# Kernel tuning notes

Measured on AMD Instinct MI355X. Metric: run time of the kernel, lower is better.

Reference implementation:

```python
import jax, jax.numpy as jnp
import numpy as np

LN_EPS = 1e-3  # keras LayerNormalization default epsilon

def setup_inputs() -> dict:
    key = jax.random.key(0)
    ks = jax.random.split(key, 8)
    B, T, N, F_in, F_out, S = 4, 4, 65536, 16, 32, 8
    E = 589824  # ~9 edges per node (8-neighbor grid + self loop)
    return {
        "water": jax.random.normal(ks[0], (B, T, N, F_in), jnp.float32),
        "static": jax.random.uniform(ks[1], (B, T, N, S), jnp.float32),
        "adj_rows": jax.random.randint(ks[2], (E,), 0, N, jnp.int32),
        "adj_cols": jax.random.randint(ks[3], (E,), 0, N, jnp.int32),
        "adj_vals": jax.random.uniform(ks[4], (E,), jnp.float32),
        "W_feat": (jax.random.normal(ks[5], (F_in, F_out), jnp.float32) * 0.1),
        "b_feat": jnp.zeros((F_out,), jnp.float32),
        "Wg1": (jax.random.normal(ks[6], (3, 1), jnp.float32) * 0.1),
        "bg1": jnp.zeros((1,), jnp.float32),
        "Wg2": (jax.random.normal(ks[7], (S - 3, 1), jnp.float32) * 0.1),
        "bg2": jnp.zeros((1,), jnp.float32),
        "ln_gamma": jnp.ones((F_out,), jnp.float32),
        "ln_beta": jnp.zeros((F_out,), jnp.float32),
        "min_gate": jnp.float32(0.1),
    }


def reference(water, static, adj_rows, adj_cols, adj_vals,
              W_feat, b_feat, Wg1, bg1, Wg2, bg2, ln_gamma, ln_beta, min_gate):
    B, T, N, F_in = water.shape
    # gated feature scaling: gate in (0,1], per (b,t,n)
    gate = jax.nn.sigmoid(static[..., :3] @ Wg1 + bg1) * jax.nn.sigmoid(static[..., 3:] @ Wg2 + bg2)
    gate = jnp.maximum(gate, min_gate)  # [B,T,N,1]
    x = (water * gate).reshape(B * T, N, F_in)
    # SpMM shared across all F_in channels and all B*T slices:
    # out[bt,n,f] = sum_{edges (n<-m)} adj_vals * x[bt,m,f]
    xs = x.transpose(1, 0, 2)                       # [N, BT, F]
    msg = adj_vals[:, None, None] * xs[adj_cols]    # [E, BT, F]
    agg = jax.ops.segment_sum(msg, adj_rows, num_segments=N)  # [N, BT, F]
    h = agg.transpose(1, 0, 2)                      # [BT, N, F]
    out = h @ W_feat + b_feat                       # [BT, N, F_out]
    out = out.reshape(B, T, N, -1)
    # layer norm over channel axis (keras default axis=-1)
    mu = out.mean(-1, keepdims=True)
    var = out.var(-1, keepdims=True)
    out = (out - mu) * jax.lax.rsqrt(var + LN_EPS) * ln_gamma + ln_beta
    # dropout is identity at inference
    return out
```

## Files before the change

### kernel.cpp

```cpp
#include <hip/hip_runtime.h>

#define BT   16
#define FIN  16
#define FOUT 32
#define CAP  32

typedef float    f32x4 __attribute__((ext_vector_type(4)));
typedef _Float16 f16x4 __attribute__((ext_vector_type(4)));
typedef _Float16 f16x8 __attribute__((ext_vector_type(8)));
typedef unsigned int u32;


__global__ __launch_bounds__(256) void zero_kernel(int4* __restrict__ p, int n4) {
    int i = blockIdx.x * 256 + threadIdx.x;
    if (i < n4) p[i] = make_int4(0, 0, 0, 0);
}


__global__ __launch_bounds__(256) void scatter_gate_kernel(
        const int* __restrict__ rows, const int* __restrict__ cols,
        const float* __restrict__ vals,
        int* __restrict__ cur, u32* __restrict__ edge_s, int E, int eb,
        const float* __restrict__ water,
        const float* __restrict__ st,
        const float* __restrict__ Wg1, const float* __restrict__ bg1,
        const float* __restrict__ Wg2, const float* __restrict__ bg2,
        const float* __restrict__ min_gate,
        _Float16* __restrict__ x, int N) {
    if (blockIdx.x < (unsigned)eb) {
        int i0 = (blockIdx.x * 256 + threadIdx.x) * 4;
        if (i0 + 4 <= E) {
            int4   r4 = *(const int4*)  (rows + i0);
            int4   c4 = *(const int4*)  (cols + i0);
            f32x4  v4 = *(const f32x4*) (vals + i0);
#pragma unroll
            for (int k = 0; k < 4; ++k) {
                int r = (&r4.x)[k];
                int pos = atomicAdd(&cur[r], 1);
                unsigned short vh = __builtin_bit_cast(unsigned short, (_Float16)v4[k]);
                if (pos < CAP)
                    edge_s[(size_t)r * CAP + pos] = ((u32)vh << 16) | (u32)(&c4.x)[k];
            }
        } else {
            for (int e = i0; e < E; ++e) {
                int r = rows[e];
                int pos = atomicAdd(&cur[r], 1);
                unsigned short vh = __builtin_bit_cast(unsigned short, (_Float16)vals[e]);
                if (pos < CAP)
                    edge_s[(size_t)r * CAP + pos] = ((u32)vh << 16) | (u32)cols[e];
            }
        }
    } else {
        int g  = blockIdx.x - eb;
        int n  = g * 16 + (threadIdx.x & 15);
        int bt = threadIdx.x >> 4;

        const f32x4* sp = (const f32x4*)(st + ((size_t)bt * N + n) * 8);
        f32x4 s0 = __builtin_nontemporal_load(sp);
        f32x4 s1 = __builtin_nontemporal_load(sp + 1);
        float g1 = s0.x * Wg1[0] + s0.y * Wg1[1] + s0.z * Wg1[2] + bg1[0];
        float g2 = s0.w * Wg2[0] + s1.x * Wg2[1] + s1.y * Wg2[2] + s1.z * Wg2[3] + s1.w * Wg2[4] + bg2[0];
        g1 = 1.f / (1.f + __expf(-g1));
        g2 = 1.f / (1.f + __expf(-g2));
        float gate = fmaxf(g1 * g2, min_gate[0]);

        const f32x4* wp = (const f32x4*)(water + ((size_t)bt * N + n) * FIN);
        f16x8 h0, h1;
#pragma unroll
        for (int k = 0; k < 4; ++k) {
            f32x4 w = __builtin_nontemporal_load(wp + k);
            w *= gate;
            f16x8& h = (k < 2) ? h0 : h1;
            int b = (k & 1) * 4;
            h[b + 0] = (_Float16)w.x; h[b + 1] = (_Float16)w.y;
            h[b + 2] = (_Float16)w.z; h[b + 3] = (_Float16)w.w;
        }
        f16x8* xp = (f16x8*)(x + ((size_t)n * BT + bt) * FIN);
        xp[0] = h0;
        xp[1] = h1;
    }
}


#define GATHER(i, off)                                                           \
    u32 p##i = ebase[e + off];                                                   \
    f16x4 g##i = xv[(size_t)(p##i & 0xffffu) * 64 + l];

#define EDGE_FMA(i)                                                              \
    do {                                                                         \
        float v = (float)__builtin_bit_cast(_Float16, (unsigned short)(p##i >> 16)); \
        acc.x += v * (float)g##i[0];                                             \
        acc.y += v * (float)g##i[1];                                             \
        acc.z += v * (float)g##i[2];                                             \
        acc.w += v * (float)g##i[3];                                             \
    } while (0)

__global__ __launch_bounds__(256) void spmm_ln_kernel(
        const _Float16* __restrict__ x,
        const int* __restrict__ cur,
        const u32* __restrict__ edge_s,
        const float* __restrict__ W,
        const float* __restrict__ bvec,
        const float* __restrict__ gamma,
        const float* __restrict__ beta,
        float* __restrict__ out, int N) {
    __shared__ float Wsh[FIN][FOUT];
    __shared__ float psh[3][FOUT];

    int t = threadIdx.x;
    Wsh[t >> 5][t & 31]       = W[t];
    Wsh[(t >> 5) + 8][t & 31] = W[t + 256];
    if (t < 32)       psh[0][t]      = bvec[t];
    else if (t < 64)  psh[1][t - 32] = gamma[t - 32];
    else if (t < 96)  psh[2][t - 64] = beta[t - 64];
    __syncthreads();

    int l = t & 63;
    int n = __builtin_amdgcn_readfirstlane(blockIdx.x * 4 + (t >> 6));
    int cnt = __builtin_amdgcn_readfirstlane(cur[n]);
    cnt = (cnt < CAP) ? cnt : CAP;
    int pcnt = (cnt + 3) & ~3;
    const u32* ebase = edge_s + (size_t)n * CAP;
    const f16x4* xv = (const f16x4*)x;

    f32x4 acc = {0.f, 0.f, 0.f, 0.f};
    int e = 0;
    for (; e + 8 <= pcnt; e += 8) {
        GATHER(0, 0) GATHER(1, 1) GATHER(2, 2) GATHER(3, 3)
        GATHER(4, 4) GATHER(5, 5) GATHER(6, 6) GATHER(7, 7)
        EDGE_FMA(0); EDGE_FMA(1); EDGE_FMA(2); EDGE_FMA(3);
        EDGE_FMA(4); EDGE_FMA(5); EDGE_FMA(6); EDGE_FMA(7);
    }
    if (e + 4 <= pcnt) {
        GATHER(0, 0) GATHER(1, 1) GATHER(2, 2) GATHER(3, 3)
        EDGE_FMA(0); EDGE_FMA(1); EDGE_FMA(2); EDGE_FMA(3);
    }

    int d = l & 3;
    float o[8];
#pragma unroll
    for (int jj = 0; jj < 8; ++jj) o[jj] = psh[0][d * 8 + jj];
#pragma unroll
    for (int q = 0; q < 4; ++q) {
        float hq[4];
        hq[0] = __shfl(acc.x, q, 4);
        hq[1] = __shfl(acc.y, q, 4);
        hq[2] = __shfl(acc.z, q, 4);
        hq[3] = __shfl(acc.w, q, 4);
#pragma unroll
        for (int m = 0; m < 4; ++m) {
            float hk = hq[m];
#pragma unroll
            for (int jj = 0; jj < 8; ++jj)
                o[jj] += hk * Wsh[q * 4 + m][d * 8 + jj];
        }
    }

    float s = 0.f, sq = 0.f;
#pragma unroll
    for (int jj = 0; jj < 8; ++jj) { s += o[jj]; sq += o[jj] * o[jj]; }
    s  += __shfl_xor(s,  1, 4);  sq += __shfl_xor(sq, 1, 4);
    s  += __shfl_xor(s,  2, 4);  sq += __shfl_xor(sq, 2, 4);
    float mu  = s * (1.f / 32.f);
    float var = sq * (1.f / 32.f) - mu * mu;
    float inv = rsqrtf(var + 1e-3f);

    f32x4 r0, r1;
#pragma unroll
    for (int jj = 0; jj < 8; ++jj) {
        float val = (o[jj] - mu) * inv * psh[1][d * 8 + jj] + psh[2][d * 8 + jj];
        if (jj < 4) r0[jj] = val;
        else        r1[jj - 4] = val;
    }
    int bt = l >> 2;
    f32x4* op = (f32x4*)(out + (size_t)bt * N * FOUT + (size_t)n * FOUT + d * 8);
    op[0] = r0;
    op[1] = r1;
}


extern "C" void kernel_launch(void* const* d_in, const int* in_sizes, int n_in,
                              void* d_out, int out_size, void* d_ws, size_t ws_size,
                              hipStream_t stream) {
    const float* water    = (const float*)d_in[0];
    const float* st       = (const float*)d_in[1];
    const int*   adj_rows = (const int*)  d_in[2];
    const int*   adj_cols = (const int*)  d_in[3];
    const float* adj_vals = (const float*)d_in[4];
    const float* W_feat   = (const float*)d_in[5];
    const float* b_feat   = (const float*)d_in[6];
    const float* Wg1      = (const float*)d_in[7];
    const float* bg1      = (const float*)d_in[8];
    const float* Wg2      = (const float*)d_in[9];
    const float* bg2      = (const float*)d_in[10];
    const float* ln_gamma = (const float*)d_in[11];
    const float* ln_beta  = (const float*)d_in[12];
    const float* min_gate = (const float*)d_in[13];
    float* out = (float*)d_out;

    int N = in_sizes[0] / (BT * FIN);
    int E = in_sizes[2];

    char* ws = (char*)d_ws;
    size_t off = 0;
    auto alloc = [&](size_t bytes) -> void* {
        off = (off + 255) & ~(size_t)255;
        void* p = ws + off;
        off += bytes;
        return p;
    };
    int*      cur    = (int*)     alloc((size_t)N * sizeof(int));
    u32*      edge_s = (u32*)     alloc((size_t)N * CAP * sizeof(u32));
    _Float16* x      = (_Float16*)alloc((size_t)N * BT * FIN * sizeof(_Float16));

    int eb = (E + 1023) / 1024;
    int gb = N / 16;
    int z4 = (N * (CAP + 1)) / 4;

    zero_kernel<<<(z4 + 255) / 256, 256, 0, stream>>>((int4*)cur, z4);
    scatter_gate_kernel<<<eb + gb, 256, 0, stream>>>(
        adj_rows, adj_cols, adj_vals, cur, edge_s, E, eb,
        water, st, Wg1, bg1, Wg2, bg2, min_gate, x, N);
    spmm_ln_kernel<<<N / 4, 256, 0, stream>>>(
        x, cur, edge_s, W_feat, b_feat, ln_gamma, ln_beta, out, N);
}
```

Measured before the change: 135.0 us.

## Zero only edge counters and gather fixed 16-edge batches with masked values

The zero kernel now clears only the per-node counters instead of also clearing the 32-slot edge table. The SpMM gather always issues 16 loads, plus a second batch of 16 when degree exceeds 16. Slots past the node's count are neutralised by forcing their value to zero, so uninitialised slots are harmless because the 16-bit column index always lands inside x. Nontemporal loads in the gate kernel become ordinary loads. The aim is to remove a large memset and raise memory-level parallelism in the gather, at the cost of wasted gathers for low-degree nodes.

```diff
diff --git a/kernel.cpp b/kernel.cpp
--- a/kernel.cpp
+++ b/kernel.cpp
@@ -56,8 +56,8 @@
         int bt = threadIdx.x >> 4;
 
         const f32x4* sp = (const f32x4*)(st + ((size_t)bt * N + n) * 8);
-        f32x4 s0 = __builtin_nontemporal_load(sp);
-        f32x4 s1 = __builtin_nontemporal_load(sp + 1);
+        f32x4 s0 = sp[0];
+        f32x4 s1 = sp[1];
         float g1 = s0.x * Wg1[0] + s0.y * Wg1[1] + s0.z * Wg1[2] + bg1[0];
         float g2 = s0.w * Wg2[0] + s1.x * Wg2[1] + s1.y * Wg2[2] + s1.z * Wg2[3] + s1.w * Wg2[4] + bg2[0];
         g1 = 1.f / (1.f + __expf(-g1));
@@ -68,7 +68,7 @@
         f16x8 h0, h1;
 #pragma unroll
         for (int k = 0; k < 4; ++k) {
-            f32x4 w = __builtin_nontemporal_load(wp + k);
+            f32x4 w = wp[k];
             w *= gate;
             f16x8& h = (k < 2) ? h0 : h1;
             int b = (k & 1) * 4;
@@ -82,18 +82,29 @@
 }
 
 
-#define GATHER(i, off)                                                           \
-    u32 p##i = ebase[e + off];                                                   \
+#define GATH16(i)                                                                \
+    u32 p##i = ebase[base + i];                                                  \
     f16x4 g##i = xv[(size_t)(p##i & 0xffffu) * 64 + l];
 
-#define EDGE_FMA(i)                                                              \
+#define FMA16(i)                                                                 \
     do {                                                                         \
-        float v = (float)__builtin_bit_cast(_Float16, (unsigned short)(p##i >> 16)); \
+        u32 hv = (base + i < cnt) ? (p##i >> 16) : 0u;          \
+        float v = (float)__builtin_bit_cast(_Float16, (unsigned short)hv);       \
         acc.x += v * (float)g##i[0];                                             \
         acc.y += v * (float)g##i[1];                                             \
         acc.z += v * (float)g##i[2];                                             \
         acc.w += v * (float)g##i[3];                                             \
     } while (0)
+
+#define BATCH16                                                                  \
+    GATH16(0)  GATH16(1)  GATH16(2)  GATH16(3)                                   \
+    GATH16(4)  GATH16(5)  GATH16(6)  GATH16(7)                                   \
+    GATH16(8)  GATH16(9)  GATH16(10) GATH16(11)                                  \
+    GATH16(12) GATH16(13) GATH16(14) GATH16(15)                                  \
+    FMA16(0);  FMA16(1);  FMA16(2);  FMA16(3);                                   \
+    FMA16(4);  FMA16(5);  FMA16(6);  FMA16(7);                                   \
+    FMA16(8);  FMA16(9);  FMA16(10); FMA16(11);                                  \
+    FMA16(12); FMA16(13); FMA16(14); FMA16(15);
 
 __global__ __launch_bounds__(256) void spmm_ln_kernel(
         const _Float16* __restrict__ x,
@@ -119,21 +130,17 @@
     int n = __builtin_amdgcn_readfirstlane(blockIdx.x * 4 + (t >> 6));
     int cnt = __builtin_amdgcn_readfirstlane(cur[n]);
     cnt = (cnt < CAP) ? cnt : CAP;
-    int pcnt = (cnt + 3) & ~3;
     const u32* ebase = edge_s + (size_t)n * CAP;
     const f16x4* xv = (const f16x4*)x;
 
     f32x4 acc = {0.f, 0.f, 0.f, 0.f};
-    int e = 0;
-    for (; e + 8 <= pcnt; e += 8) {
-        GATHER(0, 0) GATHER(1, 1) GATHER(2, 2) GATHER(3, 3)
-        GATHER(4, 4) GATHER(5, 5) GATHER(6, 6) GATHER(7, 7)
-        EDGE_FMA(0); EDGE_FMA(1); EDGE_FMA(2); EDGE_FMA(3);
-        EDGE_FMA(4); EDGE_FMA(5); EDGE_FMA(6); EDGE_FMA(7);
-    }
-    if (e + 4 <= pcnt) {
-        GATHER(0, 0) GATHER(1, 1) GATHER(2, 2) GATHER(3, 3)
-        EDGE_FMA(0); EDGE_FMA(1); EDGE_FMA(2); EDGE_FMA(3);
+    {
+        int base = 0;
+        BATCH16
+    }
+    if (cnt > 16) {
+        int base = 16;
+        BATCH16
     }
 
     int d = l & 3;
@@ -215,9 +222,8 @@
 
     int eb = (E + 1023) / 1024;
     int gb = N / 16;
-    int z4 = (N * (CAP + 1)) / 4;
-
-    zero_kernel<<<(z4 + 255) / 256, 256, 0, stream>>>((int4*)cur, z4);
+
+    zero_kernel<<<N / 1024, 256, 0, stream>>>((int4*)cur, N / 4);
     scatter_gate_kernel<<<eb + gb, 256, 0, stream>>>(
         adj_rows, adj_cols, adj_vals, cur, edge_s, E, eb,
         water, st, Wg1, bg1, Wg2, bg2, min_gate, x, N);
```

After: 129.4 us. 1.04x faster.
